# Kernel optimization log

Hardware: AMD Instinct MI355X
Metric: run time of the kernel (lower is better)

## Reference

```python
import jax, jax.numpy as jnp
import numpy as np

IN_CHN, OUT_CHN, KS = 256, 256, 3
STRIDE, PAD = 1, 1
T = 64                       # accumulator tile length
NBITS_ACC = 8                # b
NBITS_PSUM = NBITS_ACC - 3   # 5 -> Qn=-16, Qp=15
SHIFT = 4                    # shift_value for b=8 (default branch)


def _round_ste(x):
    # round with straight-through estimator (round_pass in torch code)
    return x + jax.lax.stop_gradient(jnp.round(x) - x)


def _oa(x, b):
    # bitwise overflow/wraparound correction (OA in torch code)
    mask = (1 << b) - 1
    half = 1 << (b - 1)
    qn, qp = -half, half - 1
    mid = (x >= qn) & (x <= qp)
    out = jnp.where(mid, x, 0.0)
    # torch .int() truncates toward zero; astype(int32) matches
    wrapped = (jnp.where(mid, 0.0, x).astype(jnp.int32) & mask).astype(x.dtype)
    # wrapped in [0, mask]; values > qp wrap down by 2*half (lower branch never fires)
    out3 = jnp.where(wrapped > qp, wrapped - 2.0 * half, wrapped)
    return out + out3


def setup_inputs() -> dict:
    key = jax.random.key(0)
    kx, kw = jax.random.split(key)
    x = jax.random.normal(kx, (4, IN_CHN, 56, 56), dtype=jnp.float32)
    weights = jax.random.uniform(kw, (OUT_CHN * IN_CHN * KS * KS, 1), dtype=jnp.float32) * 0.001
    return {"x": x, "weights": weights}


def reference(x, weights):
    W = weights.reshape(OUT_CHN, IN_CHN, KS, KS)
    # per-output-channel mean(|w|) scaling, detached
    scale = jax.lax.stop_gradient(jnp.mean(jnp.abs(W), axis=(1, 2, 3)))  # [Cout]
    wc = jnp.clip(W, -1.0, 1.0)
    bw = jax.lax.stop_gradient(jnp.sign(W) - wc) + wc  # sign with STE

    B, Cin, H, Wd = x.shape
    OH = (H - KS + 2 * PAD) // STRIDE + 1
    OW = (Wd - KS + 2 * PAD) // STRIDE + 1
    Kdim = Cin * KS * KS
    N = Kdim // T  # 2304 / 64 = 36 tiles, exact

    # im2col: (B, Cin*KS*KS, OH, OW), channel-major feature ordering == torch unfold
    patches = jax.lax.conv_general_dilated_patches(
        x, (KS, KS), (STRIDE, STRIDE), [(PAD, PAD), (PAD, PAD)])
    A = patches.reshape(B, Kdim, OH * OW).transpose(0, 2, 1)  # (B, L, K)
    X = bw.reshape(OUT_CHN, Kdim).T                            # (K, Cout)

    # tiled partial-sum matmul: psum[b,l,n,c] = sum_t A[b,l,n*T+t] * X[n*T+t,c]
    psum = jnp.einsum('blnt,ntc->blnc',
                      A.reshape(B, OH * OW, N, T),
                      X.reshape(N, T, OUT_CHN))

    qn = -2 ** (NBITS_PSUM - 1)
    qp = 2 ** (NBITS_PSUM - 1) - 1
    psum_q = _round_ste(jnp.clip(psum / (2.0 ** SHIFT), qn, qp))

    acc = psum_q.sum(axis=2).transpose(0, 2, 1)  # (B, Cout, L)
    out = _oa(acc, NBITS_ACC) * (2.0 ** SHIFT)
    out = out.reshape(B, OUT_CHN, OH, OW)
    return out * scale.reshape(1, -1, 1, 1)
```

## Files before the change

kernel.cpp:

```cpp
#include <hip/hip_runtime.h>

#define CIN      256
#define COUT     256
#define HWD      56
#define LSP      3136
#define BB       4
#define KDIM     2304
#define NT       36
#define BLTOT    12544

#define OFF_SCALE   0
#define OFF_HASEXC  1024
#define OFF_CNT     2048
#define OFF_EXC     38912
#define OFF_S       2398208
#define OFF_COMMON  4204544

__global__ __launch_bounds__(256)
void k_prep(const float* __restrict__ w, float* __restrict__ scale,
            int* __restrict__ has_exc, int* __restrict__ cnt, int* __restrict__ exc) {
    int c = blockIdx.x;
    int t = threadIdx.x;
    const float* wr = w + c * KDIM;
    float s = 0.f;
#pragma unroll
    for (int i = 0; i < 9; ++i) {
        int k = i * 256 + t;
        float v = wr[k];
        s += fabsf(v);
        int sg = (v > 0.f) - (v < 0.f);
        if (sg != 1) {
            int n = k >> 6;
            int ti = k & 63;
            int mag = 1 - sg;
            int idx = atomicAdd(&cnt[c * NT + n], 1);
            exc[(c * NT + n) * 64 + idx] = ti | (mag << 8);
            atomicOr(&has_exc[c], 1);
        }
    }
    __shared__ float red[256];
    red[t] = s;
    __syncthreads();
#pragma unroll
    for (int off = 128; off > 0; off >>= 1) {
        if (t < off) red[t] += red[t + off];
        __syncthreads();
    }
    if (t == 0) scale[c] = red[0] * (1.f / (float)KDIM);
}

__global__ __launch_bounds__(256)
void k_tilesum(const float* __restrict__ x, float* __restrict__ S) {
    int n = blockIdx.y;
    int bl = blockIdx.x * 256 + threadIdx.x;
    int b = bl / LSP;
    int l = bl - b * LSP;
    int oh = l / HWD;
    int ow = l - oh * HWD;
    int ihb = oh - 1, iwb = ow - 1;

    int k0 = n * 64;
    int c = k0 / 9;
    int r = k0 - 9 * c;
    const float* xc = x + (size_t)(b * CIN + c) * LSP;

    float s = 0.f;
#pragma unroll
    for (int j = 0; j < 64; ++j) {
        int kh = (r >= 3) + (r >= 6);
        int kw = r - 3 * kh;
        int ih = ihb + kh;
        int iw = iwb + kw;
        float v = 0.f;
        if ((unsigned)ih < (unsigned)HWD && (unsigned)iw < (unsigned)HWD)
            v = xc[ih * HWD + iw];
        s += v;
        if (++r == 9) { r = 0; xc += LSP; }
    }
    S[n * BLTOT + bl] = s;
}

__global__ __launch_bounds__(256)
void k_common(const float* __restrict__ S, float* __restrict__ common) {
    int bl = blockIdx.x * 256 + threadIdx.x;
    int acc = 0;
#pragma unroll
    for (int n = 0; n < NT; ++n) {
        float ps = S[n * BLTOT + bl] * 0.0625f;
        ps = fminf(fmaxf(ps, -16.f), 15.f);
        acc += (int)rintf(ps);
    }
    int w8 = ((acc + 128) & 255) - 128;
    common[bl] = (float)(w8 << 4);
}

__global__ __launch_bounds__(256)
void k_out(const float* __restrict__ x, const float* __restrict__ S,
           const float* __restrict__ common, const float* __restrict__ scale,
           const int* __restrict__ has_exc, const int* __restrict__ cnt,
           const int* __restrict__ exc, float* __restrict__ out) {
    int gid = blockIdx.x * 256 + threadIdx.x;
    int o4 = gid * 4;
    int l = o4 % LSP;
    int t = o4 / LSP;
    int c = t & 255;
    int b = t >> 8;

    float4 v;
    if (!has_exc[c]) {
        v = *(const float4*)&common[b * LSP + l];
    } else {
        float vv[4];
#pragma unroll
        for (int q = 0; q < 4; ++q) {
            int ll = l + q;
            int oh = ll / HWD, ow = ll - (ll / HWD) * HWD;
            int acc = 0;
            for (int n = 0; n < NT; ++n) {
                float ps = S[n * BLTOT + b * LSP + ll];
                int ct = cnt[c * NT + n];
                for (int e = 0; e < ct; ++e) {
                    int pk = exc[(c * NT + n) * 64 + e];
                    int ti = pk & 63;
                    int mag = pk >> 8;
                    int k = n * 64 + ti;
                    int ci = k / 9;
                    int r = k - 9 * ci;
                    int kh = r / 3;
                    int kw = r - 3 * kh;
                    int ih = oh - 1 + kh, iw = ow - 1 + kw;
                    float a = 0.f;
                    if ((unsigned)ih < (unsigned)HWD && (unsigned)iw < (unsigned)HWD)
                        a = x[(size_t)((b * CIN + ci) * HWD + ih) * HWD + iw];
                    ps -= (float)mag * a;
                }
                ps *= 0.0625f;
                ps = fminf(fmaxf(ps, -16.f), 15.f);
                acc += (int)rintf(ps);
            }
            int w8 = ((acc + 128) & 255) - 128;
            vv[q] = (float)(w8 << 4);
        }
        v = make_float4(vv[0], vv[1], vv[2], vv[3]);
    }
    float sc = scale[c];
    v.x *= sc; v.y *= sc; v.z *= sc; v.w *= sc;
    *(float4*)&out[o4] = v;
}

extern "C" void kernel_launch(void* const* d_in, const int* in_sizes, int n_in,
                              void* d_out, int out_size, void* d_ws, size_t ws_size,
                              hipStream_t stream) {
    const float* x = (const float*)d_in[0];
    const float* w = (const float*)d_in[1];
    float* out = (float*)d_out;

    char* ws = (char*)d_ws;
    float* scale   = (float*)(ws + OFF_SCALE);
    int*   has_exc = (int*)  (ws + OFF_HASEXC);
    int*   cnt     = (int*)  (ws + OFF_CNT);
    int*   exc     = (int*)  (ws + OFF_EXC);
    float* S       = (float*)(ws + OFF_S);
    float* common  = (float*)(ws + OFF_COMMON);

    hipMemsetAsync(ws + OFF_HASEXC, 0, OFF_EXC - OFF_HASEXC, stream);

    k_prep<<<COUT, 256, 0, stream>>>(w, scale, has_exc, cnt, exc);
    k_tilesum<<<dim3(BLTOT / 256, NT), 256, 0, stream>>>(x, S);
    k_common<<<BLTOT / 256, 256, 0, stream>>>(S, common);
    k_out<<<(BB * COUT * LSP) / (4 * 256), 256, 0, stream>>>(
        x, S, common, scale, has_exc, cnt, exc, out);
}
```

Before: 89.64 us.

## Fuse weight prep and tile-sum kernels into one launch, drop memset

Merges the weight-prep kernel and the tile-sum kernel into one kernel, with separate block ranges doing each job. The memset goes away because the prep blocks now zero their own counters before the atomics. The tile-sum body precomputes the nine padding masks and offsets once, then runs a fully unrolled channel-by-tap loop with fma instead of per-element index arithmetic. This removes two launches and the memset; the risk is more register pressure from the unrolled tap arrays.

Result: faster. 86.05 us (-4.0%).

```diff
diff --git a/kernel.cpp b/kernel.cpp
--- a/kernel.cpp
+++ b/kernel.cpp
@@ -8,6 +8,8 @@
 #define KDIM     2304
 #define NT       36
 #define BLTOT    12544
+#define NBX      49
+#define NTSB     (NT*NBX)
 
 #define OFF_SCALE   0
 #define OFF_HASEXC  1024
@@ -17,67 +19,88 @@
 #define OFF_COMMON  4204544
 
 __global__ __launch_bounds__(256)
-void k_prep(const float* __restrict__ w, float* __restrict__ scale,
-            int* __restrict__ has_exc, int* __restrict__ cnt, int* __restrict__ exc) {
-    int c = blockIdx.x;
-    int t = threadIdx.x;
-    const float* wr = w + c * KDIM;
-    float s = 0.f;
+void k_main(const float* __restrict__ x, const float* __restrict__ w,
+            float* __restrict__ S, float* __restrict__ scale,
+            int* __restrict__ has_exc, int* __restrict__ cnt,
+            int* __restrict__ exc) {
+    int id  = blockIdx.x;
+    int tid = threadIdx.x;
+    if (id < NTSB) {
+        int n  = id / NBX;
+        int bl = (id - n * NBX) * 256 + tid;
+        int b  = bl / LSP;
+        int l  = bl - b * LSP;
+        int oh = l / HWD;
+        int ow = l - oh * HWD;
+
+        float m[9]; int off[9];
 #pragma unroll
-    for (int i = 0; i < 9; ++i) {
-        int k = i * 256 + t;
-        float v = wr[k];
-        s += fabsf(v);
-        int sg = (v > 0.f) - (v < 0.f);
-        if (sg != 1) {
-            int n = k >> 6;
-            int ti = k & 63;
-            int mag = 1 - sg;
-            int idx = atomicAdd(&cnt[c * NT + n], 1);
-            exc[(c * NT + n) * 64 + idx] = ti | (mag << 8);
-            atomicOr(&has_exc[c], 1);
+        for (int r = 0; r < 9; ++r) {
+            int kh = r / 3, kw = r - 3 * (r / 3);
+            int ih = oh - 1 + kh, iw = ow - 1 + kw;
+            bool ok = ((unsigned)ih < (unsigned)HWD) & ((unsigned)iw < (unsigned)HWD);
+            m[r]   = ok ? 1.f : 0.f;
+            off[r] = ok ? (ih * HWD + iw) : 0;
         }
+
+        int k0 = n * 64;
+        int c0 = k0 / 9;
+        int r0 = k0 - 9 * c0;
+        const float* xc = x + (size_t)(b * CIN + c0) * LSP;
+
+        float s = 0.f;
+#pragma unroll
+        for (int r = 0; r < 9; ++r)
+            if (r >= r0) s = fmaf(m[r], xc[off[r]], s);
+        xc += LSP;
+#pragma unroll
+        for (int cc = 0; cc < 6; ++cc) {
+#pragma unroll
+            for (int r = 0; r < 9; ++r) s = fmaf(m[r], xc[off[r]], s);
+            xc += LSP;
+        }
+        if (r0 == 8) {
+#pragma unroll
+            for (int r = 0; r < 9; ++r) s = fmaf(m[r], xc[off[r]], s);
+        } else {
+#pragma unroll
+            for (int r = 0; r < 9; ++r)
+                if (r <= r0) s = fmaf(m[r], xc[off[r]], s);
+        }
+        S[n * BLTOT + bl] = s;
+    } else {
+        int c = id - NTSB;
+        if (tid < NT) cnt[c * NT + tid] = 0;
+        if (tid == 0) has_exc[c] = 0;
+        __syncthreads();
+
+        const float* wr = w + c * KDIM;
+        float s = 0.f;
+#pragma unroll
+        for (int i = 0; i < 9; ++i) {
+            int k = i * 256 + tid;
+            float v = wr[k];
+            s += fabsf(v);
+            int sg = (v > 0.f) - (v < 0.f);
+            if (sg != 1) {
+                int n  = k >> 6;
+                int ti = k & 63;
+                int mag = 1 - sg;
+                int idx = atomicAdd(&cnt[c * NT + n], 1);
+                exc[(c * NT + n) * 64 + idx] = ti | (mag << 8);
+                atomicOr(&has_exc[c], 1);
+            }
+        }
+        __shared__ float red[256];
+        red[tid] = s;
+        __syncthreads();
+#pragma unroll
+        for (int o = 128; o > 0; o >>= 1) {
+            if (tid < o) red[tid] += red[tid + o];
+            __syncthreads();
+        }
+        if (tid == 0) scale[c] = red[0] * (1.f / (float)KDIM);
     }
-    __shared__ float red[256];
-    red[t] = s;
-    __syncthreads();
-#pragma unroll
-    for (int off = 128; off > 0; off >>= 1) {
-        if (t < off) red[t] += red[t + off];
-        __syncthreads();
-    }
-    if (t == 0) scale[c] = red[0] * (1.f / (float)KDIM);
-}
-
-__global__ __launch_bounds__(256)
-void k_tilesum(const float* __restrict__ x, float* __restrict__ S) {
-    int n = blockIdx.y;
-    int bl = blockIdx.x * 256 + threadIdx.x;
-    int b = bl / LSP;
-    int l = bl - b * LSP;
-    int oh = l / HWD;
-    int ow = l - oh * HWD;
-    int ihb = oh - 1, iwb = ow - 1;
-
-    int k0 = n * 64;
-    int c = k0 / 9;
-    int r = k0 - 9 * c;
-    const float* xc = x + (size_t)(b * CIN + c) * LSP;
-
-    float s = 0.f;
-#pragma unroll
-    for (int j = 0; j < 64; ++j) {
-        int kh = (r >= 3) + (r >= 6);
-        int kw = r - 3 * kh;
-        int ih = ihb + kh;
-        int iw = iwb + kw;
-        float v = 0.f;
-        if ((unsigned)ih < (unsigned)HWD && (unsigned)iw < (unsigned)HWD)
-            v = xc[ih * HWD + iw];
-        s += v;
-        if (++r == 9) { r = 0; xc += LSP; }
-    }
-    S[n * BLTOT + bl] = s;
 }
 
 __global__ __launch_bounds__(256)
@@ -163,10 +186,7 @@
     float* S       = (float*)(ws + OFF_S);
     float* common  = (float*)(ws + OFF_COMMON);
 
-    hipMemsetAsync(ws + OFF_HASEXC, 0, OFF_EXC - OFF_HASEXC, stream);
-
-    k_prep<<<COUT, 256, 0, stream>>>(w, scale, has_exc, cnt, exc);
-    k_tilesum<<<dim3(BLTOT / 256, NT), 256, 0, stream>>>(x, S);
+    k_main<<<NTSB + COUT, 256, 0, stream>>>(x, w, S, scale, has_exc, cnt, exc);
     k_common<<<BLTOT / 256, 256, 0, stream>>>(S, common);
     k_out<<<(BB * COUT * LSP) / (4 * 256), 256, 0, stream>>>(
         x, S, common, scale, has_exc, cnt, exc, out);
```
